# Kernel tuning notes

Measured on AMD Instinct MI355X. Metric: run time of the kernel, lower is better.

## Reference

```python
import jax, jax.numpy as jnp
import numpy as np

N_CELL, N_DRUG = 8192, 4096
E_CELL, E_DRUG = 262144, 131072
D_OUT = 128


def setup_inputs() -> dict:
    key = jax.random.key(0)
    ks = jax.random.split(key, 8)
    cell_feat = jax.random.normal(ks[0], (N_CELL, N_CELL), dtype=jnp.float32)
    drug_feat = jax.random.normal(ks[1], (N_DRUG, N_DRUG), dtype=jnp.float32)
    cell_edge = jax.random.randint(ks[2], (2, E_CELL), 0, N_CELL, dtype=jnp.int64)
    drug_edge = jax.random.randint(ks[3], (2, E_DRUG), 0, N_DRUG, dtype=jnp.int64)
    W_cell = jax.random.normal(ks[4], (N_CELL, D_OUT), dtype=jnp.float32) * 0.02
    W_drug = jax.random.normal(ks[5], (N_DRUG, D_OUT), dtype=jnp.float32) * 0.02
    b_cell = jnp.zeros((D_OUT,), dtype=jnp.float32)
    b_drug = jnp.zeros((D_OUT,), dtype=jnp.float32)
    return {"cell_feat": cell_feat, "cell_edge": cell_edge, "W_cell": W_cell,
            "b_cell": b_cell, "drug_feat": drug_feat, "drug_edge": drug_edge,
            "W_drug": W_drug, "b_drug": b_drug}


def _gcn_conv(x, edge, W, b):
    """PyG GCNConv with edge_weight = x[row, col] (as in GEncoder.forward),
    add_self_loops=True, symmetric normalization."""
    N = x.shape[0]
    row, col = edge[0], edge[1]
    ew = x[row, col]                                  # [E] gathered edge weights
    loop = jnp.arange(N)
    row = jnp.concatenate([row, loop])                # [E+N] self-loops appended
    col = jnp.concatenate([col, loop])
    ew = jnp.concatenate([ew, jnp.ones((N,), x.dtype)])
    deg = jax.ops.segment_sum(ew, col, num_segments=N)
    dinv = jnp.where(deg > 0, jax.lax.rsqrt(jnp.maximum(deg, 1e-30)), 0.0)
    norm = dinv[row] * ew * dinv[col]                 # [E+N]
    h = x @ W                                         # [N, D_OUT]
    msg = norm[:, None] * h[row]                      # gather + scale
    out = jax.ops.segment_sum(msg, col, num_segments=N) + b
    return jax.nn.relu(out)


def reference(cell_feat, cell_edge, W_cell, b_cell, drug_feat, drug_edge, W_drug, b_drug):
    cell_gcn = _gcn_conv(cell_feat, cell_edge, W_cell, b_cell)
    drug_gcn = _gcn_conv(drug_feat, drug_edge, W_drug, b_drug)
    return (cell_gcn, drug_gcn)
```

## Files before the change

kernel.cpp:

```cpp
#include <hip/hip_runtime.h>
#include <stdint.h>

#define N_CELL 8192
#define N_DRUG 4096
#define E_CELL 262144
#define E_DRUG 131072
#define DOUT   128

typedef float f32x4 __attribute__((ext_vector_type(4)));
typedef short s16x8 __attribute__((ext_vector_type(8)));

#define OFF_DEG_C   0u
#define OFF_DEG_D   8192u
#define OFF_CNT_C   12288u
#define OFF_CNT_D   20480u
#define OFF_CUR_C   24576u
#define OFF_CUR_D   32768u
#define OFF_START_C 36864u
#define OFF_START_D 45312u
#define OFF_EW_C    49664u
#define OFF_EW_D    311808u
#define OFF_SROW_C  442880u
#define OFF_SROW_D  705024u
#define OFF_SCOEF_C 836096u
#define OFF_SCOEF_D 1098240u
#define OFF_H_C     1229312u
#define OFF_H_D     2277888u
#define OFF_END     2802176u
#define WT_C_BYTE   (OFF_END * 4u)
#define WT_D_BYTE   (WT_C_BYTE + 128u * 8192u * 2u)

__device__ __forceinline__ unsigned short f2bf(float f) {
    union { float f; uint32_t u; } v; v.f = f;
    uint32_t u = v.u + 0x7fffu + ((v.u >> 16) & 1u);
    return (unsigned short)(u >> 16);
}

__device__ __forceinline__ s16x8 pack8(float4 x, float4 y) {
    union { float4 f; uint32_t u[4]; } a, b;
    a.f = x; b.f = y;
    union { uint32_t u[4]; s16x8 v; } r;
    r.u[0] = __builtin_amdgcn_perm(a.u[1] + 0x8000u, a.u[0] + 0x8000u, 0x07060302u);
    r.u[1] = __builtin_amdgcn_perm(a.u[3] + 0x8000u, a.u[2] + 0x8000u, 0x07060302u);
    r.u[2] = __builtin_amdgcn_perm(b.u[1] + 0x8000u, b.u[0] + 0x8000u, 0x07060302u);
    r.u[3] = __builtin_amdgcn_perm(b.u[3] + 0x8000u, b.u[2] + 0x8000u, 0x07060302u);
    return r.v;
}

__global__ __launch_bounds__(256) void k_prep(const float* __restrict__ Wc, const float* __restrict__ Wd,
                                              unsigned short* __restrict__ wtc, unsigned short* __restrict__ wtd,
                                              float* __restrict__ ws) {
    int bid = blockIdx.x, t = threadIdx.x;
    if (bid < 144) {
        int i = bid * 256 + t;
        ws[i] = (i < 12288) ? 1.0f : 0.0f;
        return;
    }
    if (bid < 1680) {
        size_t i = (size_t)(bid - 144) * 256 + t;
        ((float4*)(ws + OFF_H_C))[i] = make_float4(0.f, 0.f, 0.f, 0.f);
        return;
    }
    int tile = bid - 1680;
    const float* W; unsigned short* wt; int K;
    if (tile < 1024) { W = Wc; wt = wtc; K = N_CELL; }
    else             { W = Wd; wt = wtd; K = N_DRUG; tile -= 1024; }
    int tk = tile >> 2, tc = tile & 3;
    __shared__ float tl[32][33];
    int c = t & 31, r8 = t >> 5;
#pragma unroll
    for (int p = 0; p < 4; ++p) {
        int row = r8 + p * 8;
        tl[row][c] = W[(size_t)(tk * 32 + row) * DOUT + tc * 32 + c];
    }
    __syncthreads();
#pragma unroll
    for (int p = 0; p < 4; ++p) {
        int c2 = r8 + p * 8;
        wt[(size_t)(tc * 32 + c2) * K + tk * 32 + c] = f2bf(tl[c][c2]);
    }
}

__global__ __launch_bounds__(256) void k_edge(const float* __restrict__ xc, const int* __restrict__ ec,
                                              const float* __restrict__ xd, const int* __restrict__ ed,
                                              float* __restrict__ ws) {
    int i = blockIdx.x * 256 + threadIdx.x;
    const float* x; const int* edges; float* ew; float* deg; int* cnt; int N, E, idx;
    if (i < E_CELL) {
        idx = i; x = xc; edges = ec; N = N_CELL; E = E_CELL;
        ew = ws + OFF_EW_C; deg = ws + OFF_DEG_C; cnt = (int*)(ws + OFF_CNT_C);
    } else {
        idx = i - E_CELL; if (idx >= E_DRUG) return;
        x = xd; edges = ed; N = N_DRUG; E = E_DRUG;
        ew = ws + OFF_EW_D; deg = ws + OFF_DEG_D; cnt = (int*)(ws + OFF_CNT_D);
    }
    int r = edges[idx], c = edges[E + idx];
    float w = x[(size_t)r * N + c];
    ew[idx] = w;
    unsafeAtomicAdd(&deg[c], w);
    atomicAdd(&cnt[c], 1);
}

__global__ __launch_bounds__(256) void k_scan2(float* ws) {
    int bid = blockIdx.x, t = threadIdx.x;
    if (bid < 48) {
        int i = bid * 256 + t;
        float d = ws[i];
        ws[i] = d > 0.f ? rsqrtf(fmaxf(d, 1e-30f)) : 0.f;
        return;
    }
    const int* cnt; int* start; int N, chunk;
    if (bid == 48) { cnt = (const int*)(ws + OFF_CNT_C); start = (int*)(ws + OFF_START_C); N = N_CELL; chunk = 32; }
    else           { cnt = (const int*)(ws + OFF_CNT_D); start = (int*)(ws + OFF_START_D); N = N_DRUG; chunk = 16; }
    __shared__ int sums[256];
    int base = t * chunk;
    int s = 0;
    for (int j = 0; j < chunk; ++j) s += cnt[base + j];
    sums[t] = s; __syncthreads();
    for (int off = 1; off < 256; off <<= 1) {
        int v = (t >= off) ? sums[t - off] : 0;
        __syncthreads();
        sums[t] += v;
        __syncthreads();
    }
    int run = sums[t] - s;
    for (int j = 0; j < chunk; ++j) { start[base + j] = run; run += cnt[base + j]; }
    if (t == 255) start[N] = run;
}

__global__ __launch_bounds__(256) void k_fill(const int* __restrict__ ec, const int* __restrict__ ed,
                                              float* __restrict__ ws) {
    int i = blockIdx.x * 256 + threadIdx.x;
    const int* edges; const float* ew; const float* dinv; const int* start;
    int* cur; int* srow; float* scoef; int E, idx;
    if (i < E_CELL) {
        idx = i; edges = ec; E = E_CELL;
        ew = ws + OFF_EW_C; dinv = ws + OFF_DEG_C; start = (const int*)(ws + OFF_START_C);
        cur = (int*)(ws + OFF_CUR_C); srow = (int*)(ws + OFF_SROW_C); scoef = ws + OFF_SCOEF_C;
    } else {
        idx = i - E_CELL; if (idx >= E_DRUG) return;
        edges = ed; E = E_DRUG;
        ew = ws + OFF_EW_D; dinv = ws + OFF_DEG_D; start = (const int*)(ws + OFF_START_D);
        cur = (int*)(ws + OFF_CUR_D); srow = (int*)(ws + OFF_SROW_D); scoef = ws + OFF_SCOEF_D;
    }
    int r = edges[idx], c = edges[E + idx];
    float coef = dinv[r] * ew[idx] * dinv[c];
    int slot = start[c] + atomicAdd(&cur[c], 1);
    srow[slot] = r;
    scoef[slot] = coef;
}

__global__ __launch_bounds__(256, 6) void k_gemm(const float* __restrict__ xc, const float* __restrict__ xd,
                                                 const unsigned short* __restrict__ wtc,
                                                 const unsigned short* __restrict__ wtd,
                                                 float* __restrict__ ws) {
    int bid = blockIdx.x, t = threadIdx.x;
    const float* x; const unsigned short* wt; float* h; int K, mt, ch;
    if (bid < 2048) { x = xc; wt = wtc; h = ws + OFF_H_C; K = N_CELL; mt = bid >> 3; ch = bid & 7; }
    else { int b = bid - 2048; x = xd; wt = wtd; h = ws + OFF_H_D; K = N_DRUG; mt = b >> 2; ch = b & 3; }
    int k0 = ch << 10;

    __shared__ alignas(16) unsigned short As[2][32][72];
    int lane = t & 63, wv = t >> 6;
    int l15 = lane & 15, l4 = lane >> 4;

    f32x4 acc[2][2] = {};

    int srow = t >> 3, sseg = t & 7;
    const float* abase = x + (size_t)(mt * 32 + srow) * K + k0 + sseg * 8;
    const unsigned short* bb = wt + (size_t)(wv * 32 + l15) * K + k0 + l4 * 8;
    const unsigned short* bb1 = bb + (size_t)16 * K;

    float4 X0, X1;

#define LOADA(KT) { const float4* _p = (const float4*)(abase + (size_t)(KT) * 64); \
                    X0 = _p[0]; X1 = _p[1]; }
#define WRITEA(BUF) { *(s16x8*)&As[BUF][srow][sseg * 8] = pack8(X0, X1); }

    LOADA(0);
    WRITEA(0);
    LOADA(1);
    __syncthreads();

#pragma unroll 1
    for (int kt = 0; kt < 16; ++kt) {
        s16x8 bq00 = *(const s16x8*)(bb  + (size_t)kt * 64);
        s16x8 bq01 = *(const s16x8*)(bb  + (size_t)kt * 64 + 32);
        s16x8 bq10 = *(const s16x8*)(bb1 + (size_t)kt * 64);
        s16x8 bq11 = *(const s16x8*)(bb1 + (size_t)kt * 64 + 32);
        if (kt < 15) {
            WRITEA((kt + 1) & 1);
            if (kt < 14) LOADA(kt + 2);
        }
        int bf = kt & 1;
        {
            s16x8 a0 = *(const s16x8*)&As[bf][l15][l4 * 8];
            s16x8 a1 = *(const s16x8*)&As[bf][16 + l15][l4 * 8];
            acc[0][0] = __builtin_amdgcn_mfma_f32_16x16x32_bf16(a0, bq00, acc[0][0], 0, 0, 0);
            acc[0][1] = __builtin_amdgcn_mfma_f32_16x16x32_bf16(a0, bq10, acc[0][1], 0, 0, 0);
            acc[1][0] = __builtin_amdgcn_mfma_f32_16x16x32_bf16(a1, bq00, acc[1][0], 0, 0, 0);
            acc[1][1] = __builtin_amdgcn_mfma_f32_16x16x32_bf16(a1, bq10, acc[1][1], 0, 0, 0);
        }
        {
            s16x8 a0 = *(const s16x8*)&As[bf][l15][32 + l4 * 8];
            s16x8 a1 = *(const s16x8*)&As[bf][16 + l15][32 + l4 * 8];
            acc[0][0] = __builtin_amdgcn_mfma_f32_16x16x32_bf16(a0, bq01, acc[0][0], 0, 0, 0);
            acc[0][1] = __builtin_amdgcn_mfma_f32_16x16x32_bf16(a0, bq11, acc[0][1], 0, 0, 0);
            acc[1][0] = __builtin_amdgcn_mfma_f32_16x16x32_bf16(a1, bq01, acc[1][0], 0, 0, 0);
            acc[1][1] = __builtin_amdgcn_mfma_f32_16x16x32_bf16(a1, bq11, acc[1][1], 0, 0, 0);
        }
        __syncthreads();
    }
#undef LOADA
#undef WRITEA
#pragma unroll
    for (int m = 0; m < 2; ++m)
#pragma unroll
        for (int n = 0; n < 2; ++n) {
            int col = wv * 32 + n * 16 + l15;
            int row = mt * 32 + m * 16 + l4 * 4;
#pragma unroll
            for (int j = 0; j < 4; ++j)
                unsafeAtomicAdd(&h[(size_t)(row + j) * DOUT + col], acc[m][n][j]);
        }
}

__global__ __launch_bounds__(256) void k_gather(const float* __restrict__ ws,
                                                const float* __restrict__ bc, const float* __restrict__ bd,
                                                float* __restrict__ out) {
    int wv = threadIdx.x >> 6, lane = threadIdx.x & 63;
    int g = blockIdx.x * 4 + wv;
    const float* h; const int* srow; const float* scoef; const int* start; const float* dinv;
    const float* bvec; float* outp; int node;
    if (g < N_CELL) {
        node = g; h = ws + OFF_H_C; srow = (const int*)(ws + OFF_SROW_C); scoef = ws + OFF_SCOEF_C;
        start = (const int*)(ws + OFF_START_C); dinv = ws + OFF_DEG_C; bvec = bc; outp = out;
    } else {
        node = g - N_CELL; if (node >= N_DRUG) return;
        h = ws + OFF_H_D; srow = (const int*)(ws + OFF_SROW_D); scoef = ws + OFF_SCOEF_D;
        start = (const int*)(ws + OFF_START_D); dinv = ws + OFF_DEG_D; bvec = bd;
        outp = out + (size_t)N_CELL * DOUT;
    }
    float di = dinv[node], sc = di * di;
    float2 v = ((const float2*)(h + (size_t)node * DOUT))[lane];
    float ax = sc * v.x, ay = sc * v.y;
    int s0 = start[node], s1 = start[node + 1];
    int e = s0;
    for (; e + 3 < s1; e += 4) {
        int r0 = srow[e];     float c0 = scoef[e];
        int r1 = srow[e + 1]; float c1 = scoef[e + 1];
        int r2 = srow[e + 2]; float c2 = scoef[e + 2];
        int r3 = srow[e + 3]; float c3 = scoef[e + 3];
        float2 u0 = ((const float2*)(h + (size_t)r0 * DOUT))[lane];
        float2 u1 = ((const float2*)(h + (size_t)r1 * DOUT))[lane];
        float2 u2 = ((const float2*)(h + (size_t)r2 * DOUT))[lane];
        float2 u3 = ((const float2*)(h + (size_t)r3 * DOUT))[lane];
        ax += c0 * u0.x + c1 * u1.x + c2 * u2.x + c3 * u3.x;
        ay += c0 * u0.y + c1 * u1.y + c2 * u2.y + c3 * u3.y;
    }
    for (; e < s1; ++e) {
        int r = srow[e]; float cf = scoef[e];
        float2 u = ((const float2*)(h + (size_t)r * DOUT))[lane];
        ax += cf * u.x; ay += cf * u.y;
    }
    float2 bb = ((const float2*)bvec)[lane];
    ax = fmaxf(ax + bb.x, 0.f);
    ay = fmaxf(ay + bb.y, 0.f);
    float2 o; o.x = ax; o.y = ay;
    ((float2*)outp)[(size_t)node * 64 + lane] = o;
}

extern "C" void kernel_launch(void* const* d_in, const int* in_sizes, int n_in,
                              void* d_out, int out_size, void* d_ws, size_t ws_size,
                              hipStream_t stream) {
    const float* cell_feat = (const float*)d_in[0];
    const int*   cell_edge = (const int*)d_in[1];
    const float* W_cell    = (const float*)d_in[2];
    const float* b_cell    = (const float*)d_in[3];
    const float* drug_feat = (const float*)d_in[4];
    const int*   drug_edge = (const int*)d_in[5];
    const float* W_drug    = (const float*)d_in[6];
    const float* b_drug    = (const float*)d_in[7];
    float* out = (float*)d_out;
    float* ws  = (float*)d_ws;
    unsigned short* wtc = (unsigned short*)((char*)d_ws + WT_C_BYTE);
    unsigned short* wtd = (unsigned short*)((char*)d_ws + WT_D_BYTE);

    k_prep<<<3216, 256, 0, stream>>>(W_cell, W_drug, wtc, wtd, ws);
    k_edge<<<(E_CELL + E_DRUG) / 256, 256, 0, stream>>>(cell_feat, cell_edge, drug_feat, drug_edge, ws);
    k_scan2<<<50, 256, 0, stream>>>(ws);
    k_fill<<<1536, 256, 0, stream>>>(cell_edge, drug_edge, ws);
    k_gemm<<<2560, 256, 0, stream>>>(cell_feat, drug_feat, wtc, wtd, ws);
    k_gather<<<3072, 256, 0, stream>>>(ws, b_cell, b_drug, out);
}
```

Measured before the change: 237.1 us.

## Halve split-K factor and replace atomic accumulation with partial buffers plus reduce

The projection GEMM now splits K into 4 chunks for cell and 2 for drug instead of 8 and 4. Each block runs a 32-step K loop, and the grid drops to 1280 blocks. When the workspace is large enough, each split writes its partial tile to its own buffer with plain stores instead of float atomics. A new reduce kernel then sums the partials into H. This removes atomic contention and the partial-wave tail, at the cost of extra partial-buffer traffic, one more launch and less parallelism per block.

```diff
diff --git a/kernel.cpp b/kernel.cpp
--- a/kernel.cpp
+++ b/kernel.cpp
@@ -29,6 +29,9 @@
 #define OFF_END     2802176u
 #define WT_C_BYTE   (OFF_END * 4u)
 #define WT_D_BYTE   (WT_C_BYTE + 128u * 8192u * 2u)
+#define PART_C_BYTE 14354432u
+#define PART_D_BYTE 31131648u
+#define PART_END    35325952u
 
 __device__ __forceinline__ unsigned short f2bf(float f) {
     union { float f; uint32_t u; } v; v.f = f;
@@ -153,12 +156,19 @@
 __global__ __launch_bounds__(256, 6) void k_gemm(const float* __restrict__ xc, const float* __restrict__ xd,
                                                  const unsigned short* __restrict__ wtc,
                                                  const unsigned short* __restrict__ wtd,
-                                                 float* __restrict__ ws) {
+                                                 float* __restrict__ ws,
+                                                 float* __restrict__ partC, float* __restrict__ partD,
+                                                 int usePart) {
     int bid = blockIdx.x, t = threadIdx.x;
-    const float* x; const unsigned short* wt; float* h; int K, mt, ch;
-    if (bid < 2048) { x = xc; wt = wtc; h = ws + OFF_H_C; K = N_CELL; mt = bid >> 3; ch = bid & 7; }
-    else { int b = bid - 2048; x = xd; wt = wtd; h = ws + OFF_H_D; K = N_DRUG; mt = b >> 2; ch = b & 3; }
-    int k0 = ch << 10;
+    const float* x; const unsigned short* wt; float* hp; float* part; int K, mt, ch; size_t pstride;
+    if (bid < 1024) {
+        x = xc; wt = wtc; hp = ws + OFF_H_C; part = partC; K = N_CELL;
+        mt = bid >> 2; ch = bid & 3; pstride = (size_t)N_CELL * DOUT;
+    } else {
+        int b = bid - 1024; x = xd; wt = wtd; hp = ws + OFF_H_D; part = partD; K = N_DRUG;
+        mt = b >> 1; ch = b & 1; pstride = (size_t)N_DRUG * DOUT;
+    }
+    int k0 = ch * 2048;
 
     __shared__ alignas(16) unsigned short As[2][32][72];
     int lane = t & 63, wv = t >> 6;
@@ -183,14 +193,14 @@
     __syncthreads();
 
 #pragma unroll 1
-    for (int kt = 0; kt < 16; ++kt) {
+    for (int kt = 0; kt < 32; ++kt) {
         s16x8 bq00 = *(const s16x8*)(bb  + (size_t)kt * 64);
         s16x8 bq01 = *(const s16x8*)(bb  + (size_t)kt * 64 + 32);
         s16x8 bq10 = *(const s16x8*)(bb1 + (size_t)kt * 64);
         s16x8 bq11 = *(const s16x8*)(bb1 + (size_t)kt * 64 + 32);
-        if (kt < 15) {
+        if (kt < 31) {
             WRITEA((kt + 1) & 1);
-            if (kt < 14) LOADA(kt + 2);
+            if (kt < 30) LOADA(kt + 2);
         }
         int bf = kt & 1;
         {
@@ -213,16 +223,47 @@
     }
 #undef LOADA
 #undef WRITEA
-#pragma unroll
-    for (int m = 0; m < 2; ++m)
-#pragma unroll
-        for (int n = 0; n < 2; ++n) {
-            int col = wv * 32 + n * 16 + l15;
-            int row = mt * 32 + m * 16 + l4 * 4;
-#pragma unroll
-            for (int j = 0; j < 4; ++j)
-                unsafeAtomicAdd(&h[(size_t)(row + j) * DOUT + col], acc[m][n][j]);
-        }
+    if (usePart) {
+        float* dst = part + (size_t)ch * pstride;
+#pragma unroll
+        for (int m = 0; m < 2; ++m)
+#pragma unroll
+            for (int n = 0; n < 2; ++n) {
+                int col = wv * 32 + n * 16 + l15;
+                int row = mt * 32 + m * 16 + l4 * 4;
+#pragma unroll
+                for (int j = 0; j < 4; ++j)
+                    dst[(size_t)(row + j) * DOUT + col] = acc[m][n][j];
+            }
+    } else {
+#pragma unroll
+        for (int m = 0; m < 2; ++m)
+#pragma unroll
+            for (int n = 0; n < 2; ++n) {
+                int col = wv * 32 + n * 16 + l15;
+                int row = mt * 32 + m * 16 + l4 * 4;
+#pragma unroll
+                for (int j = 0; j < 4; ++j)
+                    unsafeAtomicAdd(&hp[(size_t)(row + j) * DOUT + col], acc[m][n][j]);
+            }
+    }
+}
+
+__global__ __launch_bounds__(256) void k_reduce(const float* __restrict__ partC,
+                                                const float* __restrict__ partD,
+                                                float* __restrict__ ws) {
+    int bid = blockIdx.x, t = threadIdx.x;
+    if (bid < 1024) {
+        size_t i = (size_t)bid * 256 + t;
+        const f32x4* p = (const f32x4*)partC;
+        f32x4 s = p[i] + p[i + 262144] + p[i + 2 * 262144] + p[i + 3 * 262144];
+        ((f32x4*)(ws + OFF_H_C))[i] = s;
+    } else {
+        size_t i = (size_t)(bid - 1024) * 256 + t;
+        const f32x4* p = (const f32x4*)partD;
+        f32x4 s = p[i] + p[i + 131072];
+        ((f32x4*)(ws + OFF_H_D))[i] = s;
+    }
 }
 
 __global__ __launch_bounds__(256) void k_gather(const float* __restrict__ ws,
@@ -285,11 +326,15 @@
     float* ws  = (float*)d_ws;
     unsigned short* wtc = (unsigned short*)((char*)d_ws + WT_C_BYTE);
     unsigned short* wtd = (unsigned short*)((char*)d_ws + WT_D_BYTE);
+    float* partC = (float*)((char*)d_ws + PART_C_BYTE);
+    float* partD = (float*)((char*)d_ws + PART_D_BYTE);
+    int usePart = (ws_size >= (size_t)PART_END) ? 1 : 0;
 
     k_prep<<<3216, 256, 0, stream>>>(W_cell, W_drug, wtc, wtd, ws);
     k_edge<<<(E_CELL + E_DRUG) / 256, 256, 0, stream>>>(cell_feat, cell_edge, drug_feat, drug_edge, ws);
     k_scan2<<<50, 256, 0, stream>>>(ws);
     k_fill<<<1536, 256, 0, stream>>>(cell_edge, drug_edge, ws);
-    k_gemm<<<2560, 256, 0, stream>>>(cell_feat, drug_feat, wtc, wtd, ws);
+    k_gemm<<<1280, 256, 0, stream>>>(cell_feat, drug_feat, wtc, wtd, ws, partC, partD, usePart);
+    if (usePart) k_reduce<<<1536, 256, 0, stream>>>(partC, partD, ws);
     k_gather<<<3072, 256, 0, stream>>>(ws, b_cell, b_drug, out);
 }
```

Measured after the change: 240.6 us. About the same (+1.5%).
